# Kernel tuning notes

Hardware: AMD Instinct MI355X
Metric: run time of the kernel (lower is better)

## Reference

```python
import jax, jax.numpy as jnp
import numpy as np

EMB = 1024
HEADS = 16
HEAD_DIM = EMB // HEADS


def setup_inputs() -> dict:
    key = jax.random.key(0)
    ks = jax.random.split(key, 6)
    B, T, D = 4, 2048, EMB
    s = 1.0 / np.sqrt(D)
    return {
        "x": jax.random.normal(ks[0], (B, T, D), dtype=jnp.float32),
        "Wq": jax.random.normal(ks[1], (D, D), dtype=jnp.float32) * s,
        "Wk": jax.random.normal(ks[2], (D, D), dtype=jnp.float32) * s,
        "Wv": jax.random.normal(ks[3], (D, D), dtype=jnp.float32) * s,
        "Wo": jax.random.normal(ks[4], (D, D), dtype=jnp.float32) * s,
        "bo": jax.random.normal(ks[5], (D,), dtype=jnp.float32) * 0.01,
    }


def reference(x, Wq, Wk, Wv, Wo, bo):
    B, T, D = x.shape
    H, Hd = HEADS, HEAD_DIM
    # torch Linear: x @ W.T ; here W stored [out,in]
    def heads(W):
        return (x @ W.T).reshape(B, T, H, Hd).transpose(0, 2, 1, 3)  # [B,H,T,Hd]
    Q, K, V = heads(Wq), heads(Wk), heads(Wv)
    scores = jnp.einsum("bhqd,bhkd->bhqk", Q, K) / np.sqrt(Hd)
    causal = jnp.triu(jnp.ones((T, T), dtype=bool), k=1)
    scores = jnp.where(causal, -jnp.inf, scores)
    weights = jax.nn.softmax(scores, axis=-1)  # dropout rate 0 -> identity
    ctx = jnp.einsum("bhqk,bhkd->bhqd", weights, V)
    ctx = ctx.transpose(0, 2, 1, 3).reshape(B, T, D)
    return ctx @ Wo.T + bo
```

## Files before the change

kernel.cpp:

```cpp
#include <hip/hip_runtime.h>

typedef short bf16x8 __attribute__((ext_vector_type(8)));
typedef float f32x4 __attribute__((ext_vector_type(4)));
typedef unsigned short u16;
typedef unsigned int u32;

__device__ __forceinline__ u16 f2b(float x) {
  union { float f; u32 u; } c; c.f = x;
  u32 r = (c.u + 0x7FFFu + ((c.u >> 16) & 1u)) >> 16;
  return (u16)r;
}

__device__ __forceinline__ float fexp2(float x) {
  return __builtin_amdgcn_exp2f(x);
}

__device__ __forceinline__ void glds16(const void* g, void* l) {
  __builtin_amdgcn_global_load_lds(
      (const __attribute__((address_space(1))) u32*)g,
      (__attribute__((address_space(3))) u32*)l, 16, 0, 0);
}

__global__ void cvt_all(const float* __restrict__ x, const float* __restrict__ Wq,
                        const float* __restrict__ Wk, const float* __restrict__ Wv,
                        const float* __restrict__ Wo, u16* __restrict__ xb,
                        u16* __restrict__ wqkvb, u16* __restrict__ wob, float qscale) {
  const int i = blockIdx.x * blockDim.x + threadIdx.x;
  const float* src;
  u16* dst;
  float scale = 1.0f;
  int off;
  if (i < 2097152) {
    src = x; dst = xb; off = i;
  } else {
    const int j = i - 2097152;
    const int wsel = j >> 18;
    off = j & 262143;
    if (wsel == 0)      { src = Wq; dst = wqkvb;            scale = qscale; }
    else if (wsel == 1) { src = Wk; dst = wqkvb + 1048576; }
    else if (wsel == 2) { src = Wv; dst = wqkvb + 2097152; }
    else                { src = Wo; dst = wob; }
  }
  float4 v = reinterpret_cast<const float4*>(src)[off];
  ushort4 o;
  o.x = f2b(v.x * scale); o.y = f2b(v.y * scale);
  o.z = f2b(v.z * scale); o.w = f2b(v.w * scale);
  reinterpret_cast<ushort4*>(dst)[off] = o;
}

template<int MODE>
__global__ __launch_bounds__(256, 2)
void gemm2(const u16* __restrict__ A, const u16* __restrict__ Bm,
           u16* __restrict__ Cq, u16* __restrict__ Ck, u16* __restrict__ Cvt,
           float* __restrict__ Cf, const float* __restrict__ bias) {
  constexpr int K = 1024, NKT = 32;
  __shared__ __attribute__((aligned(16))) u16 lds[3][12288];
  const int tid = threadIdx.x;
  const int w = tid >> 6, l = tid & 63;
  const int wm = w >> 1, wn = w & 1;
  const int lr = l & 15, lg = l >> 4;
  const int brow = blockIdx.x * 128;
  const int bcol = blockIdx.y * 256;
  const u16* Ab = A + (size_t)brow * K;
  const u16* Bb = Bm + (size_t)bcol * K;

  int gA[2], gB[4];
#pragma unroll
  for (int i = 0; i < 2; ++i) {
    const int q = i * 256 + tid, r = q >> 2, s = q & 3;
    gA[i] = r * K + ((s ^ (r & 3)) * 8);
  }
#pragma unroll
  for (int i = 0; i < 4; ++i) {
    const int q = i * 256 + tid, r = q >> 2, s = q & 3;
    gB[i] = r * K + ((s ^ (r & 3)) * 8);
  }
  const int ldsw = w * 512;

  int a_off[4], b_off[8];
#pragma unroll
  for (int m = 0; m < 4; ++m) {
    const int row = wm * 64 + m * 16 + lr;
    a_off[m] = (row * 4 + (lg ^ (lr & 3))) * 8;
  }
#pragma unroll
  for (int n = 0; n < 8; ++n) {
    const int row = wn * 128 + n * 16 + lr;
    b_off[n] = 4096 + (row * 4 + (lg ^ (lr & 3))) * 8;
  }

  f32x4 acc[4][8] = {};

#pragma unroll
  for (int t = 0; t < 2; ++t) {
#pragma unroll
    for (int i = 0; i < 2; ++i) glds16(Ab + gA[i] + t * 32, &lds[t][i * 2048 + ldsw]);
#pragma unroll
    for (int i = 0; i < 4; ++i) glds16(Bb + gB[i] + t * 32, &lds[t][4096 + i * 2048 + ldsw]);
  }
  asm volatile("s_waitcnt vmcnt(6)" ::: "memory");
  asm volatile("s_barrier" ::: "memory");

  int bi = 0;
  for (int kt = 0; kt < NKT; ++kt) {
    const u16* Lb = lds[bi];
    bf16x8 a[4], b[8];
#pragma unroll
    for (int m = 0; m < 4; ++m) a[m] = *reinterpret_cast<const bf16x8*>(&Lb[a_off[m]]);
#pragma unroll
    for (int n = 0; n < 8; ++n) b[n] = *reinterpret_cast<const bf16x8*>(&Lb[b_off[n]]);
    if (kt + 2 < NKT) {
      const int bs = (bi + 2 >= 3) ? (bi - 1) : (bi + 2);
      const int ko = (kt + 2) * 32;
#pragma unroll
      for (int i = 0; i < 2; ++i) glds16(Ab + gA[i] + ko, &lds[bs][i * 2048 + ldsw]);
#pragma unroll
      for (int i = 0; i < 4; ++i) glds16(Bb + gB[i] + ko, &lds[bs][4096 + i * 2048 + ldsw]);
    }
    __builtin_amdgcn_s_setprio(1);
#pragma unroll
    for (int m = 0; m < 4; ++m)
#pragma unroll
      for (int n = 0; n < 8; ++n)
        acc[m][n] = __builtin_amdgcn_mfma_f32_16x16x32_bf16(a[m], b[n], acc[m][n], 0, 0, 0);
    __builtin_amdgcn_s_setprio(0);
    if (kt + 1 < NKT) {
      if (kt + 2 < NKT) asm volatile("s_waitcnt vmcnt(6)" ::: "memory");
      else              asm volatile("s_waitcnt vmcnt(0)" ::: "memory");
    }
    asm volatile("s_barrier" ::: "memory");
    bi = (bi + 1 >= 3) ? 0 : bi + 1;
  }

  if (MODE == 0) {
    const int seg = blockIdx.y >> 2;
    const int cbase = (blockIdx.y & 3) * 256;
    if (seg < 2) {
      u16* dst = (seg == 0) ? Cq : Ck;
#pragma unroll
      for (int m = 0; m < 4; ++m) {
        const size_t r0 = (size_t)(brow + wm * 64 + m * 16 + lg * 4);
#pragma unroll
        for (int n = 0; n < 8; ++n) {
          const int c = cbase + wn * 128 + n * 16 + lr;
#pragma unroll
          for (int j = 0; j < 4; ++j)
            dst[(r0 + j) * 1024 + c] = f2b(acc[m][n][j]);
        }
      }
    } else {
#pragma unroll
      for (int n = 0; n < 8; ++n) {
        const int c = cbase + wn * 128 + n * 16 + lr;
        const int hh = c >> 6, dd = c & 63;
#pragma unroll
        for (int m = 0; m < 4; ++m) {
          const int r0 = brow + wm * 64 + m * 16 + lg * 4;
#pragma unroll
          for (int j = 0; j < 4; ++j) {
            const int r = r0 + j;
            const int bt = r >> 11, tt = r & 2047;
            Cvt[((size_t)((bt * 16 + hh) * 64 + dd)) * 2048 + tt] = f2b(acc[m][n][j]);
          }
        }
      }
    }
  } else {
#pragma unroll
    for (int m = 0; m < 4; ++m) {
      const size_t r0 = (size_t)(brow + wm * 64 + m * 16 + lg * 4);
#pragma unroll
      for (int n = 0; n < 8; ++n) {
        const int c = bcol + wn * 128 + n * 16 + lr;
        const float bv = bias[c];
#pragma unroll
        for (int j = 0; j < 4; ++j)
          Cf[(r0 + j) * 1024 + c] = acc[m][n][j] + bv;
      }
    }
  }
}

__global__ __launch_bounds__(256, 3)
void attn_kernel(const u16* __restrict__ qb, const u16* __restrict__ kb,
                 const u16* __restrict__ vt, u16* __restrict__ ctx) {
  __shared__ __attribute__((aligned(16))) u16 Ks[2][64 * 72];
  __shared__ __attribute__((aligned(16))) u16 Vs[2][64 * 72];
  __shared__ __attribute__((aligned(16))) u16 Ps[4 * 32 * 64];
  const int bid = blockIdx.x;
  const int qt = 15 - (bid >> 6);
  const int bh = bid & 63;
  const int bb = bh >> 4, h = bh & 15;
  const int tid = threadIdx.x, w = tid >> 6, l = tid & 63;
  const int lr = l & 15, lg = l >> 4;
  const int Qw = qt * 128 + w * 32;
  const int kvr = tid >> 3;
  const int kvc = (tid & 7) * 8;

  bf16x8 qf[2][2];
#pragma unroll
  for (int mi = 0; mi < 2; ++mi)
#pragma unroll
    for (int kc = 0; kc < 2; ++kc)
      qf[mi][kc] = *reinterpret_cast<const bf16x8*>(
          &qb[(size_t)(bb * 2048 + Qw + mi * 16 + lr) * 1024 + h * 64 + kc * 32 + lg * 8]);

  f32x4 oacc[2][4] = {};
  float lsum[2][4] = {};

  const int ntiles = 2 * qt + 2;

  bf16x8 kr[2], vr[2];
#pragma unroll
  for (int it = 0; it < 2; ++it) {
    kr[it] = *reinterpret_cast<const bf16x8*>(
        &kb[(size_t)(bb * 2048 + it * 32 + kvr) * 1024 + h * 64 + kvc]);
    vr[it] = *reinterpret_cast<const bf16x8*>(
        &vt[(size_t)(bh * 64 + it * 32 + kvr) * 2048 + kvc]);
  }
#pragma unroll
  for (int it = 0; it < 2; ++it) {
    *reinterpret_cast<bf16x8*>(&Ks[0][(it * 32 + kvr) * 72 + kvc]) = kr[it];
    *reinterpret_cast<bf16x8*>(&Vs[0][(it * 32 + kvr) * 72 + kvc]) = vr[it];
  }
  __syncthreads();
#pragma unroll
  for (int it = 0; it < 2; ++it) {
    kr[it] = *reinterpret_cast<const bf16x8*>(
        &kb[(size_t)(bb * 2048 + 64 + it * 32 + kvr) * 1024 + h * 64 + kvc]);
    vr[it] = *reinterpret_cast<const bf16x8*>(
        &vt[(size_t)(bh * 64 + it * 32 + kvr) * 2048 + 64 + kvc]);
  }

  for (int t = 0; t < ntiles; ++t) {
    const int c0 = t * 64;
    const int cur = t & 1;

    if (c0 < Qw + 32) {
      const bool diag = (c0 + 63 > Qw);

      f32x4 sacc[2][4] = {};
      __builtin_amdgcn_s_setprio(1);
#pragma unroll
      for (int kc = 0; kc < 2; ++kc)
#pragma unroll
        for (int nj = 0; nj < 4; ++nj) {
          bf16x8 kf = *reinterpret_cast<const bf16x8*>(
              &Ks[cur][(nj * 16 + lr) * 72 + kc * 32 + lg * 8]);
#pragma unroll
          for (int mi = 0; mi < 2; ++mi)
            sacc[mi][nj] = __builtin_amdgcn_mfma_f32_16x16x32_bf16(qf[mi][kc], kf, sacc[mi][nj], 0, 0, 0);
        }
      __builtin_amdgcn_s_setprio(0);

#pragma unroll
      for (int mi = 0; mi < 2; ++mi) {
        if (diag) {
#pragma unroll
          for (int nj = 0; nj < 4; ++nj) {
            const int col = c0 + nj * 16 + lr;
#pragma unroll
            for (int j = 0; j < 4; ++j) {
              const int row = Qw + mi * 16 + lg * 4 + j;
              if (col > row) sacc[mi][nj][j] = -1e30f;
            }
          }
        }
#pragma unroll
        for (int nj = 0; nj < 4; ++nj) {
          const int cchunk = nj * 2 + (lr >> 3);
          const int coff = lr & 7;
#pragma unroll
          for (int j = 0; j < 4; ++j) {
            const float p = fexp2(sacc[mi][nj][j]);
            lsum[mi][j] += p;
            const int rowP = mi * 16 + lg * 4 + j;
            Ps[w * 2048 + rowP * 64 + ((cchunk ^ (rowP & 7)) * 8) + coff] = f2b(p);
          }
        }
      }

      __builtin_amdgcn_s_setprio(1);
#pragma unroll
      for (int kc = 0; kc < 2; ++kc) {
        bf16x8 pf[2];
#pragma unroll
        for (int mi = 0; mi < 2; ++mi) {
          const int rowP = mi * 16 + lr;
          const int cj = kc * 4 + lg;
          pf[mi] = *reinterpret_cast<const bf16x8*>(
              &Ps[w * 2048 + rowP * 64 + ((cj ^ (rowP & 7)) * 8)]);
        }
#pragma unroll
        for (int nd = 0; nd < 4; ++nd) {
          bf16x8 vf = *reinterpret_cast<const bf16x8*>(
              &Vs[cur][(nd * 16 + lr) * 72 + kc * 32 + lg * 8]);
#pragma unroll
          for (int mi = 0; mi < 2; ++mi)
            oacc[mi][nd] = __builtin_amdgcn_mfma_f32_16x16x32_bf16(pf[mi], vf, oacc[mi][nd], 0, 0, 0);
        }
      }
      __builtin_amdgcn_s_setprio(0);
    }

    if (t + 1 < ntiles) {
#pragma unroll
      for (int it = 0; it < 2; ++it) {
        *reinterpret_cast<bf16x8*>(&Ks[cur ^ 1][(it * 32 + kvr) * 72 + kvc]) = kr[it];
        *reinterpret_cast<bf16x8*>(&Vs[cur ^ 1][(it * 32 + kvr) * 72 + kvc]) = vr[it];
      }
    }
    __syncthreads();
    if (t + 2 < ntiles) {
      const int c0n = c0 + 128;
#pragma unroll
      for (int it = 0; it < 2; ++it) {
        kr[it] = *reinterpret_cast<const bf16x8*>(
            &kb[(size_t)(bb * 2048 + c0n + it * 32 + kvr) * 1024 + h * 64 + kvc]);
        vr[it] = *reinterpret_cast<const bf16x8*>(
            &vt[(size_t)(bh * 64 + it * 32 + kvr) * 2048 + c0n + kvc]);
      }
    }
  }

#pragma unroll
  for (int mi = 0; mi < 2; ++mi) {
#pragma unroll
    for (int x = 1; x < 16; x <<= 1)
#pragma unroll
      for (int j = 0; j < 4; ++j) lsum[mi][j] += __shfl_xor(lsum[mi][j], x, 64);
#pragma unroll
    for (int j = 0; j < 4; ++j) {
      const float inv = 1.0f / lsum[mi][j];
      const size_t r = (size_t)(bb * 2048 + Qw + mi * 16 + lg * 4 + j);
#pragma unroll
      for (int nd = 0; nd < 4; ++nd)
        ctx[r * 1024 + h * 64 + nd * 16 + lr] = f2b(oacc[mi][nd][j] * inv);
    }
  }
}

extern "C" void kernel_launch(void* const* d_in, const int* in_sizes, int n_in,
                              void* d_out, int out_size, void* d_ws, size_t ws_size,
                              hipStream_t stream) {
  const float* x = (const float*)d_in[0];
  const float* Wq = (const float*)d_in[1];
  const float* Wk = (const float*)d_in[2];
  const float* Wv = (const float*)d_in[3];
  const float* Wo = (const float*)d_in[4];
  const float* bo = (const float*)d_in[5];
  float* out = (float*)d_out;

  char* ws = (char*)d_ws;
  u16* xb = (u16*)(ws);
  u16* qb = (u16*)(ws + (16u << 20));
  u16* kb = (u16*)(ws + (32u << 20));
  u16* vtb = (u16*)(ws + (64u << 20));
  u16* wqkvb = (u16*)(ws + (80u << 20));
  u16* wob = (u16*)(ws + (88u << 20));

  const float qscale = 0.125f * 1.4426950408889634f;
  cvt_all<<<12288, 256, 0, stream>>>(x, Wq, Wk, Wv, Wo, xb, wqkvb, wob, qscale);

  gemm2<0><<<dim3(64, 12), 256, 0, stream>>>(xb, wqkvb, qb, kb, vtb, nullptr, nullptr);
  attn_kernel<<<1024, 256, 0, stream>>>(qb, kb, vtb, xb);
  gemm2<1><<<dim3(64, 4), 256, 0, stream>>>(xb, wob, nullptr, nullptr, nullptr, out, bo);
}
```

Measured before the change: 157.8 us.

## Use 256x256 GEMM tiles with 8 waves and 4-stage ping-pong pipeline

Replaces the 128x256, 4-wave GEMM with a 256x256 tile computed by 512 threads (2x4 waves, each 128x64). The K loop becomes a 4-stage LDS ring buffer with split halves: A and B loads are interleaved with two MFMA phases, separated by barriers and setprio. The aim is more data reuse per tile, deeper prefetch, and better overlap of loads with MFMA. The cost is more LDS per block (128KB), extra barriers per iteration, and half as many blocks, which risks lower occupancy and a smaller grid for the output projection GEMM (128 blocks).

```diff
diff --git a/kernel.cpp b/kernel.cpp
--- a/kernel.cpp
+++ b/kernel.cpp
@@ -49,87 +49,102 @@
 }
 
 template<int MODE>
-__global__ __launch_bounds__(256, 2)
-void gemm2(const u16* __restrict__ A, const u16* __restrict__ Bm,
+__global__ __launch_bounds__(512, 2)
+void gemm3(const u16* __restrict__ A, const u16* __restrict__ Bm,
            u16* __restrict__ Cq, u16* __restrict__ Ck, u16* __restrict__ Cvt,
            float* __restrict__ Cf, const float* __restrict__ bias) {
   constexpr int K = 1024, NKT = 32;
-  __shared__ __attribute__((aligned(16))) u16 lds[3][12288];
+  __shared__ __attribute__((aligned(16))) u16 lds[4][16384];
   const int tid = threadIdx.x;
   const int w = tid >> 6, l = tid & 63;
-  const int wm = w >> 1, wn = w & 1;
+  const int wm = w >> 2, wn = w & 3;
   const int lr = l & 15, lg = l >> 4;
-  const int brow = blockIdx.x * 128;
+  const int brow = blockIdx.x * 256;
   const int bcol = blockIdx.y * 256;
   const u16* Ab = A + (size_t)brow * K;
   const u16* Bb = Bm + (size_t)bcol * K;
 
-  int gA[2], gB[4];
+  int gsrc[2];
 #pragma unroll
   for (int i = 0; i < 2; ++i) {
-    const int q = i * 256 + tid, r = q >> 2, s = q & 3;
-    gA[i] = r * K + ((s ^ (r & 3)) * 8);
-  }
-#pragma unroll
-  for (int i = 0; i < 4; ++i) {
-    const int q = i * 256 + tid, r = q >> 2, s = q & 3;
-    gB[i] = r * K + ((s ^ (r & 3)) * 8);
-  }
-  const int ldsw = w * 512;
-
-  int a_off[4], b_off[8];
-#pragma unroll
-  for (int m = 0; m < 4; ++m) {
-    const int row = wm * 64 + m * 16 + lr;
-    a_off[m] = (row * 4 + (lg ^ (lr & 3))) * 8;
-  }
-#pragma unroll
-  for (int n = 0; n < 8; ++n) {
-    const int row = wn * 128 + n * 16 + lr;
-    b_off[n] = 4096 + (row * 4 + (lg ^ (lr & 3))) * 8;
-  }
-
-  f32x4 acc[4][8] = {};
-
-#pragma unroll
-  for (int t = 0; t < 2; ++t) {
-#pragma unroll
-    for (int i = 0; i < 2; ++i) glds16(Ab + gA[i] + t * 32, &lds[t][i * 2048 + ldsw]);
-#pragma unroll
-    for (int i = 0; i < 4; ++i) glds16(Bb + gB[i] + t * 32, &lds[t][4096 + i * 2048 + ldsw]);
-  }
-  asm volatile("s_waitcnt vmcnt(6)" ::: "memory");
+    const int q = i * 512 + tid, r = q >> 2, p = q & 3;
+    gsrc[i] = r * K + ((p ^ ((r >> 1) & 3)) * 8);
+  }
+
+  int a_off[8], b_off[4];
+#pragma unroll
+  for (int m = 0; m < 8; ++m) {
+    const int row = wm * 128 + m * 16 + lr;
+    a_off[m] = row * 32 + ((lg ^ ((row >> 1) & 3)) * 8);
+  }
+#pragma unroll
+  for (int n = 0; n < 4; ++n) {
+    const int row = wn * 64 + n * 16 + lr;
+    b_off[n] = 8192 + row * 32 + ((lg ^ ((row >> 1) & 3)) * 8);
+  }
+
+  f32x4 acc[8][4] = {};
+
+#pragma unroll
+  for (int t = 0; t < 3; ++t) {
+    glds16(Ab + gsrc[0] + t * 32, &lds[t][tid * 8]);
+    glds16(Ab + gsrc[1] + t * 32, &lds[t][4096 + tid * 8]);
+    glds16(Bb + gsrc[0] + t * 32, &lds[t][8192 + tid * 8]);
+    glds16(Bb + gsrc[1] + t * 32, &lds[t][12288 + tid * 8]);
+  }
+  asm volatile("s_waitcnt vmcnt(8)" ::: "memory");
   asm volatile("s_barrier" ::: "memory");
 
-  int bi = 0;
   for (int kt = 0; kt < NKT; ++kt) {
-    const u16* Lb = lds[bi];
-    bf16x8 a[4], b[8];
+    const u16* Lb = lds[kt & 3];
+    u16* Sb = lds[(kt + 3) & 3];
+    const int ko = (kt + 3) * 32;
+    const bool st = (kt + 3 < NKT);
+
+    bf16x8 a[4], b[4];
 #pragma unroll
     for (int m = 0; m < 4; ++m) a[m] = *reinterpret_cast<const bf16x8*>(&Lb[a_off[m]]);
 #pragma unroll
-    for (int n = 0; n < 8; ++n) b[n] = *reinterpret_cast<const bf16x8*>(&Lb[b_off[n]]);
-    if (kt + 2 < NKT) {
-      const int bs = (bi + 2 >= 3) ? (bi - 1) : (bi + 2);
-      const int ko = (kt + 2) * 32;
-#pragma unroll
-      for (int i = 0; i < 2; ++i) glds16(Ab + gA[i] + ko, &lds[bs][i * 2048 + ldsw]);
-#pragma unroll
-      for (int i = 0; i < 4; ++i) glds16(Bb + gB[i] + ko, &lds[bs][4096 + i * 2048 + ldsw]);
-    }
+    for (int n = 0; n < 4; ++n) b[n] = *reinterpret_cast<const bf16x8*>(&Lb[b_off[n]]);
+    if (st) {
+      glds16(Ab + gsrc[0] + ko, &Sb[tid * 8]);
+      glds16(Ab + gsrc[1] + ko, &Sb[4096 + tid * 8]);
+    }
+    asm volatile("s_barrier" ::: "memory");
+    asm volatile("s_waitcnt lgkmcnt(0)" ::: "memory");
+    __builtin_amdgcn_sched_barrier(0);
     __builtin_amdgcn_s_setprio(1);
 #pragma unroll
     for (int m = 0; m < 4; ++m)
 #pragma unroll
-      for (int n = 0; n < 8; ++n)
+      for (int n = 0; n < 4; ++n)
         acc[m][n] = __builtin_amdgcn_mfma_f32_16x16x32_bf16(a[m], b[n], acc[m][n], 0, 0, 0);
     __builtin_amdgcn_s_setprio(0);
+    asm volatile("s_barrier" ::: "memory");
+
+    bf16x8 a2[4];
+#pragma unroll
+    for (int m = 0; m < 4; ++m) a2[m] = *reinterpret_cast<const bf16x8*>(&Lb[a_off[m + 4]]);
+    if (st) {
+      glds16(Bb + gsrc[0] + ko, &Sb[8192 + tid * 8]);
+      glds16(Bb + gsrc[1] + ko, &Sb[12288 + tid * 8]);
+    }
     if (kt + 1 < NKT) {
-      if (kt + 2 < NKT) asm volatile("s_waitcnt vmcnt(6)" ::: "memory");
-      else              asm volatile("s_waitcnt vmcnt(0)" ::: "memory");
+      if (st)                 asm volatile("s_waitcnt vmcnt(8)" ::: "memory");
+      else if (kt + 2 < NKT)  asm volatile("s_waitcnt vmcnt(4)" ::: "memory");
+      else                    asm volatile("s_waitcnt vmcnt(0)" ::: "memory");
     }
     asm volatile("s_barrier" ::: "memory");
-    bi = (bi + 1 >= 3) ? 0 : bi + 1;
+    asm volatile("s_waitcnt lgkmcnt(0)" ::: "memory");
+    __builtin_amdgcn_sched_barrier(0);
+    __builtin_amdgcn_s_setprio(1);
+#pragma unroll
+    for (int m = 0; m < 4; ++m)
+#pragma unroll
+      for (int n = 0; n < 4; ++n)
+        acc[m + 4][n] = __builtin_amdgcn_mfma_f32_16x16x32_bf16(a2[m], b[n], acc[m + 4][n], 0, 0, 0);
+    __builtin_amdgcn_s_setprio(0);
+    if (kt + 1 < NKT) asm volatile("s_barrier" ::: "memory");
   }
 
   if (MODE == 0) {
@@ -138,11 +153,11 @@
     if (seg < 2) {
       u16* dst = (seg == 0) ? Cq : Ck;
 #pragma unroll
-      for (int m = 0; m < 4; ++m) {
-        const size_t r0 = (size_t)(brow + wm * 64 + m * 16 + lg * 4);
-#pragma unroll
-        for (int n = 0; n < 8; ++n) {
-          const int c = cbase + wn * 128 + n * 16 + lr;
+      for (int m = 0; m < 8; ++m) {
+        const size_t r0 = (size_t)(brow + wm * 128 + m * 16 + lg * 4);
+#pragma unroll
+        for (int n = 0; n < 4; ++n) {
+          const int c = cbase + wn * 64 + n * 16 + lr;
 #pragma unroll
           for (int j = 0; j < 4; ++j)
             dst[(r0 + j) * 1024 + c] = f2b(acc[m][n][j]);
@@ -150,12 +165,12 @@
       }
     } else {
 #pragma unroll
-      for (int n = 0; n < 8; ++n) {
-        const int c = cbase + wn * 128 + n * 16 + lr;
+      for (int n = 0; n < 4; ++n) {
+        const int c = cbase + wn * 64 + n * 16 + lr;
         const int hh = c >> 6, dd = c & 63;
 #pragma unroll
-        for (int m = 0; m < 4; ++m) {
-          const int r0 = brow + wm * 64 + m * 16 + lg * 4;
+        for (int m = 0; m < 8; ++m) {
+          const int r0 = brow + wm * 128 + m * 16 + lg * 4;
 #pragma unroll
           for (int j = 0; j < 4; ++j) {
             const int r = r0 + j;
@@ -167,11 +182,11 @@
     }
   } else {
 #pragma unroll
-    for (int m = 0; m < 4; ++m) {
-      const size_t r0 = (size_t)(brow + wm * 64 + m * 16 + lg * 4);
-#pragma unroll
-      for (int n = 0; n < 8; ++n) {
-        const int c = bcol + wn * 128 + n * 16 + lr;
+    for (int m = 0; m < 8; ++m) {
+      const size_t r0 = (size_t)(brow + wm * 128 + m * 16 + lg * 4);
+#pragma unroll
+      for (int n = 0; n < 4; ++n) {
+        const int c = bcol + wn * 64 + n * 16 + lr;
         const float bv = bias[c];
 #pragma unroll
         for (int j = 0; j < 4; ++j)
@@ -362,7 +377,7 @@
   const float qscale = 0.125f * 1.4426950408889634f;
   cvt_all<<<12288, 256, 0, stream>>>(x, Wq, Wk, Wv, Wo, xb, wqkvb, wob, qscale);
 
-  gemm2<0><<<dim3(64, 12), 256, 0, stream>>>(xb, wqkvb, qb, kb, vtb, nullptr, nullptr);
+  gemm3<0><<<dim3(32, 12), 512, 0, stream>>>(xb, wqkvb, qb, kb, vtb, nullptr, nullptr);
   attn_kernel<<<1024, 256, 0, stream>>>(qb, kb, vtb, xb);
-  gemm2<1><<<dim3(64, 4), 256, 0, stream>>>(xb, wob, nullptr, nullptr, nullptr, out, bo);
-}
+  gemm3<1><<<dim3(32, 4), 512, 0, stream>>>(xb, wob, nullptr, nullptr, nullptr, out, bo);
+}
```

Result: slower. 175.4 us (+11.1%).
